# Performance work log

Hardware: AMD Instinct MI355X
Metric: run time of the kernel (lower is better)

Reference implementation:

```python
import jax, jax.numpy as jnp
import numpy as np

B, T = 64, 512
OBS, DM, DS, NL = 115, 128, 8, 3
EMB, NA, H1 = 16, 19, 256


def _ln(x, g, b, eps=1e-5):
    m = jnp.mean(x, -1, keepdims=True)
    v = jnp.mean((x - m) ** 2, -1, keepdims=True)
    return (x - m) * jax.lax.rsqrt(v + eps) * g + b


def _s6(x, h, lng, lnb, w_ig, w_dt, b_dt, a_log, w_b, w_c, d_par, w_out):
    # x: [B,T,DM], h: [B,DM,DS]
    xn = _ln(x, lng, lnb)
    xp = xn @ w_ig.T                               # [B,T,2*DM]
    x_in, z = xp[..., :DM], xp[..., DM:]
    dt = jax.nn.softplus(x_in @ w_dt.T + b_dt)     # [B,T,DM]
    A = -jnp.exp(a_log)                            # [DM,DS]
    bt = x_in @ w_b.T                              # [B,T,DS]
    ct = x_in @ w_c.T                              # [B,T,DS]
    dA = jnp.exp(dt[..., None] * A)                # [B,T,DM,DS]
    upd = (dt * x_in)[..., None] * bt[:, :, None, :]  # [B,T,DM,DS]

    def step(hc, inp):
        dA_t, u_t, c_t = inp
        hn = dA_t * hc + u_t                       # [B,DM,DS]
        y = jnp.einsum('bds,bs->bd', hn, c_t)      # [B,DM]
        return hn, y

    h_f, ys = jax.lax.scan(
        step, h,
        (jnp.swapaxes(dA, 0, 1), jnp.swapaxes(upd, 0, 1), jnp.swapaxes(ct, 0, 1)))
    y = jnp.swapaxes(ys, 0, 1)                     # [B,T,DM]
    ssm = y * jax.nn.silu(z) + x_in * d_par
    return x + ssm @ w_out.T, h_f.reshape(h_f.shape[0], -1)


def _forward(prev_actions, obs, h0, enc_w1, enc_b1, enc_g1, enc_bb1, enc_w2, enc_b2,
             enc_g2, enc_bb2, emb, proj_w, proj_b, proj_g, proj_bb,
             m_ln_g, m_ln_b, m_w_ig, m_w_dt, m_b_dt, m_a_log, m_w_b, m_w_c, m_d, m_w_out,
             fn_g, fn_b, pol_w1, pol_b1, pol_g, pol_bb, pol_w2, pol_b2):
    # MLP encoder: Linear -> LN -> SiLU -> Linear -> LN (final norm)
    e = jax.nn.silu(_ln(obs @ enc_w1.T + enc_b1, enc_g1, enc_bb1))
    e = _ln(e @ enc_w2.T + enc_b2, enc_g2, enc_bb2)
    pa = emb[prev_actions]                         # [B,T,EMB]
    x = jnp.concatenate([e, pa], -1) @ proj_w.T + proj_b
    x = jax.nn.silu(_ln(x, proj_g, proj_bb))
    for i in range(NL):
        x, _ = _s6(x, h0[i].reshape(-1, DM, DS), m_ln_g[i], m_ln_b[i], m_w_ig[i],
                   m_w_dt[i], m_b_dt[i], m_a_log[i], m_w_b[i], m_w_c[i], m_d[i], m_w_out[i])
    x = _ln(x, fn_g, fn_b)
    p = jax.nn.silu(_ln(x @ pol_w1.T + pol_b1, pol_g, pol_bb))
    return p @ pol_w2.T + pol_b2                   # [B,T,NA] policy logits


def setup_inputs() -> dict:
    key = jax.random.key(0)
    ks = iter(jax.random.split(key, 64))
    def n(shape, s=0.05):
        return jax.random.normal(next(ks), shape, dtype=jnp.float32) * s
    return {
        'obs': jax.random.normal(next(ks), (B, T, OBS), dtype=jnp.float32),
        'h0': jnp.zeros((NL, B, DM * DS), jnp.float32),
        'enc_w1': n((H1, OBS)), 'enc_b1': jnp.zeros((H1,)),
        'enc_g1': jnp.ones((H1,)), 'enc_bb1': jnp.zeros((H1,)),
        'enc_w2': n((DM, H1)), 'enc_b2': jnp.zeros((DM,)),
        'enc_g2': jnp.ones((DM,)), 'enc_bb2': jnp.zeros((DM,)),
        'emb': n((NA + 1, EMB), 1.0),
        'proj_w': n((DM, DM + EMB)), 'proj_b': jnp.zeros((DM,)),
        'proj_g': jnp.ones((DM,)), 'proj_bb': jnp.zeros((DM,)),
        'm_ln_g': jnp.ones((NL, DM)), 'm_ln_b': jnp.zeros((NL, DM)),
        'm_w_ig': n((NL, 2 * DM, DM)), 'm_w_dt': n((NL, DM, DM)),
        'm_b_dt': jnp.zeros((NL, DM)),
        'm_a_log': jax.random.uniform(next(ks), (NL, DM, DS), minval=-3.0, maxval=-1.0, dtype=jnp.float32),
        'm_w_b': n((NL, DS, DM)), 'm_w_c': n((NL, DS, DM)),
        'm_d': jnp.ones((NL, DM)), 'm_w_out': n((NL, DM, DM)),
        'fn_g': jnp.ones((DM,)), 'fn_b': jnp.zeros((DM,)),
        'pol_w1': n((DM, DM)), 'pol_b1': jnp.zeros((DM,)),
        'pol_g': jnp.ones((DM,)), 'pol_bb': jnp.zeros((DM,)),
        'pol_w2': n((NA, DM)), 'pol_b2': jnp.zeros((NA,)),
        'prev_actions': jax.random.randint(next(ks), (B, T), 0, NA + 1),
    }


def reference(obs, h0, enc_w1, enc_b1, enc_g1, enc_bb1, enc_w2, enc_b2, enc_g2, enc_bb2,
              emb, proj_w, proj_b, proj_g, proj_bb, m_ln_g, m_ln_b, m_w_ig, m_w_dt,
              m_b_dt, m_a_log, m_w_b, m_w_c, m_d, m_w_out, fn_g, fn_b, pol_w1, pol_b1,
              pol_g, pol_bb, pol_w2, pol_b2, prev_actions):
    return _forward(prev_actions, obs, h0, enc_w1, enc_b1, enc_g1, enc_bb1, enc_w2,
                    enc_b2, enc_g2, enc_bb2, emb, proj_w, proj_b, proj_g, proj_bb,
                    m_ln_g, m_ln_b, m_w_ig, m_w_dt, m_b_dt, m_a_log, m_w_b, m_w_c,
                    m_d, m_w_out, fn_g, fn_b, pol_w1, pol_b1, pol_g, pol_bb, pol_w2, pol_b2)
```

## Files before the change

### kernel.cpp

```cpp
#include <hip/hip_runtime.h>
#include <math.h>

#define BB 64
#define TT 512
#define OBSD 115
#define DMD 128
#define DSD 8
#define NLD 3
#define EMBD 16
#define NAD 19
#define H1D 256
#define NTOK (BB*TT)
#define SSEG 32
#define TSEG (TT/SSEG)

typedef unsigned short ushort_t;
typedef __attribute__((ext_vector_type(8))) short short8;
typedef __attribute__((ext_vector_type(4))) float f32x4;

__device__ __forceinline__ float silu_f(float x){ return x / (1.f + __expf(-x)); }
__device__ __forceinline__ float softplus_f(float x){
  return fmaxf(x, 0.f) + log1pf(__expf(-fabsf(x)));
}
__device__ __forceinline__ ushort_t f2bf(float x){
  unsigned u = __float_as_uint(x);
  unsigned r = (u + 0x7fffu + ((u >> 16) & 1u)) >> 16;
  return (ushort_t)r;
}
__device__ __forceinline__ float b2f(ushort_t x){
  return __uint_as_float(((unsigned)x) << 16);
}
#define MFMA(a,b,c) __builtin_amdgcn_mfma_f32_16x16x32_bf16((a),(b),(c),0,0,0)
#define LOG2E 1.44269504f

template<int D, int SV>
__device__ __forceinline__ void ln32(const float* s_val, float* s_mr, int tid){
  const int t = tid >> 3, part = tid & 7;
  float s = 0.f, s2 = 0.f;
  #pragma unroll
  for (int j = part; j < D; j += 8){ float v = s_val[t*SV + j]; s += v; s2 = fmaf(v, v, s2); }
  s += __shfl_xor(s, 1, 64); s2 += __shfl_xor(s2, 1, 64);
  s += __shfl_xor(s, 2, 64); s2 += __shfl_xor(s2, 2, 64);
  s += __shfl_xor(s, 4, 64); s2 += __shfl_xor(s2, 4, 64);
  if (part == 0){
    float m = s * (1.f/(float)D);
    s_mr[t*2] = m;
    s_mr[t*2+1] = rsqrtf(s2 * (1.f/(float)D) - m*m + 1e-5f);
  }
}

struct PJob { const float* src; ushort_t* dst; int N; int K; int Kpad; int rowofs; int Nw; };
struct PJobs { PJob j[20]; };

__global__ __launch_bounds__(256) void k_prep(PJobs P){
  const int job = blockIdx.x >> 2;
  const int sub = blockIdx.x & 3;
  PJob pj = P.j[job];
  const int elems = pj.Nw * pj.Kpad;
  for (int idx = sub*256 + threadIdx.x; idx < elems; idx += 4*256){
    int n = idx / pj.Kpad;
    int k = idx - n*pj.Kpad;
    float v = (n < pj.N && k < pj.K) ? pj.src[(size_t)n*pj.K + k] : 0.f;
    pj.dst[(size_t)(pj.rowofs + n)*pj.Kpad + k] = f2bf(v);
  }
}

__global__ __launch_bounds__(256) void k_enc1(
    const float* __restrict__ obs, const ushort_t* __restrict__ w1b,
    const float* __restrict__ b1, const float* __restrict__ g1,
    const float* __restrict__ bb1, ushort_t* __restrict__ e1)
{
  __shared__ __align__(16) char sm[34048];
  float*    s_val = (float*)sm;
  ushort_t* s_a   = (ushort_t*)sm;
  float*    s_mr  = (float*)(sm + 33792);
  const int tok0 = blockIdx.x * 32;
  const int tid = threadIdx.x;
  const int lane = tid & 63, w = tid >> 6;
  const int q = lane >> 4, cn = lane & 15;
  const int m0 = (w & 1) * 16, nh = w >> 1;

  for (int e = tid; e < 32*16; e += 256){
    int t = e >> 4, kc = e & 15;
    const float* op = obs + (size_t)(tok0 + t)*OBSD;
    short8 v;
    #pragma unroll
    for (int j = 0; j < 8; j++){
      int k = kc*8 + j;
      v[j] = (short)f2bf(k < OBSD ? op[k] : 0.f);
    }
    *(short8*)&s_a[t*136 + kc*8] = v;
  }
  __syncthreads();

  short8 af[4];
  #pragma unroll
  for (int ks = 0; ks < 4; ks++)
    af[ks] = *(const short8*)&s_a[(m0 + cn)*136 + ks*32 + q*8];
  __syncthreads();

  #pragma unroll
  for (int nt = 0; nt < 8; nt++){
    const int n0 = (nh*8 + nt) * 16;
    f32x4 acc = {0.f,0.f,0.f,0.f};
    #pragma unroll
    for (int ks = 0; ks < 4; ks++){
      short8 bf = *(const short8*)&w1b[(size_t)(n0 + cn)*128 + ks*32 + q*8];
      acc = MFMA(af[ks], bf, acc);
    }
    float bias = b1[n0 + cn];
    #pragma unroll
    for (int r = 0; r < 4; r++)
      s_val[(m0 + q*4 + r)*264 + n0 + cn] = acc[r] + bias;
  }
  __syncthreads();

  ln32<256,264>(s_val, s_mr, tid);
  __syncthreads();
  for (int e = tid; e < 32*256; e += 256){
    int t = e >> 8, c = e & 255;
    float v = (s_val[t*264 + c] - s_mr[t*2]) * s_mr[t*2+1] * g1[c] + bb1[c];
    e1[(size_t)(tok0 + t)*256 + c] = f2bf(silu_f(v));
  }
}

__global__ __launch_bounds__(256) void k_enc2p(
    const ushort_t* __restrict__ e1, const ushort_t* __restrict__ w2b,
    const float* __restrict__ b2, const float* __restrict__ g2,
    const float* __restrict__ bb2,
    const float* __restrict__ emb, const int* __restrict__ pact,
    const ushort_t* __restrict__ pwb, const float* __restrict__ pb,
    const float* __restrict__ pg, const float* __restrict__ pbb,
    float* __restrict__ X,
    const float* __restrict__ lng, const float* __restrict__ lnb,
    const ushort_t* __restrict__ wigb, const ushort_t* __restrict__ wdbcb,
    const float* __restrict__ bdt,
    ushort_t* __restrict__ XINb, ushort_t* __restrict__ Zb,
    ushort_t* __restrict__ DTb, ushort_t* __restrict__ BTu, ushort_t* __restrict__ CTu,
    const float* __restrict__ alog0,
    float* __restrict__ HLOC, float* __restrict__ PPR)
{
  __shared__ __align__(16) char sm[28928];
  float*    s_val = (float*)sm;
  ushort_t* s_xin = (ushort_t*)sm;
  ushort_t* s_dt  = (ushort_t*)(sm + 8704);
  ushort_t* s_a   = (ushort_t*)(sm + 17408);
  ushort_t* s_btc = (ushort_t*)(sm + 28160);
  float*    s_mr  = (float*)(sm + 28672);

  const int tok0 = blockIdx.x * 32;
  const int bidx = blockIdx.x >> 4;
  const int ch   = blockIdx.x & 15;
  const int tid = threadIdx.x;
  const int lane = tid & 63, w = tid >> 6;
  const int q = lane >> 4, cn = lane & 15;
  const int m0 = (w & 1) * 16, nh = w >> 1;

  for (int e = tid; e < 32*32; e += 256){
    int t = e >> 5, k = e & 31;
    float v = 0.f;
    if (k < EMBD){ int a = pact[tok0 + t]; v = emb[(size_t)a*EMBD + k]; }
    s_a[t*168 + 128 + k] = f2bf(v);
  }
  {
    short8 af[8];
    #pragma unroll
    for (int ks = 0; ks < 8; ks++)
      af[ks] = *(const short8*)&e1[(size_t)(tok0 + m0 + cn)*256 + ks*32 + q*8];
    #pragma unroll
    for (int nt = 0; nt < 4; nt++){
      const int n0 = (nh*4 + nt) * 16;
      f32x4 acc = {0.f,0.f,0.f,0.f};
      #pragma unroll
      for (int ks = 0; ks < 8; ks++){
        short8 bf = *(const short8*)&w2b[(size_t)(n0 + cn)*256 + ks*32 + q*8];
        acc = MFMA(af[ks], bf, acc);
      }
      float bias = b2[n0 + cn];
      #pragma unroll
      for (int r = 0; r < 4; r++)
        s_val[(m0 + q*4 + r)*136 + n0 + cn] = acc[r] + bias;
    }
  }
  __syncthreads();

  ln32<128,136>(s_val, s_mr, tid);
  __syncthreads();
  for (int e = tid; e < 32*128; e += 256){
    int t = e >> 7, c = e & 127;
    float v = (s_val[t*136 + c] - s_mr[t*2]) * s_mr[t*2+1] * g2[c] + bb2[c];
    s_a[t*168 + c] = f2bf(v);
  }
  __syncthreads();

  {
    short8 af2[5];
    #pragma unroll
    for (int ks = 0; ks < 5; ks++)
      af2[ks] = *(const short8*)&s_a[(m0 + cn)*168 + ks*32 + q*8];
    #pragma unroll
    for (int nt = 0; nt < 4; nt++){
      const int n0 = (nh*4 + nt) * 16;
      f32x4 acc = {0.f,0.f,0.f,0.f};
      #pragma unroll
      for (int ks = 0; ks < 5; ks++){
        short8 bf = *(const short8*)&pwb[(size_t)(n0 + cn)*160 + ks*32 + q*8];
        acc = MFMA(af2[ks], bf, acc);
      }
      float bias = pb[n0 + cn];
      #pragma unroll
      for (int r = 0; r < 4; r++)
        s_val[(m0 + q*4 + r)*136 + n0 + cn] = acc[r] + bias;
    }
  }
  __syncthreads();

  ln32<128,136>(s_val, s_mr, tid);
  __syncthreads();
  for (int e = tid; e < 32*128; e += 256){
    int t = e >> 7, c = e & 127;
    float v = (s_val[t*136 + c] - s_mr[t*2]) * s_mr[t*2+1] * pg[c] + pbb[c];
    v = silu_f(v);
    X[(size_t)tok0*128 + e] = v;
    s_val[t*136 + c] = v;
  }
  __syncthreads();

  ln32<128,136>(s_val, s_mr, tid);
  __syncthreads();
  for (int e = tid; e < 32*128; e += 256){
    int t = e >> 7, c = e & 127;
    float v = (s_val[t*136 + c] - s_mr[t*2]) * s_mr[t*2+1] * lng[c] + lnb[c];
    s_a[t*168 + c] = f2bf(v);
  }
  __syncthreads();

  {
    short8 af[4];
    #pragma unroll
    for (int ks = 0; ks < 4; ks++)
      af[ks] = *(const short8*)&s_a[(m0 + cn)*168 + ks*32 + q*8];
    #pragma unroll
    for (int nt = 0; nt < 8; nt++){
      const int n0 = (nh*8 + nt) * 16;
      f32x4 acc = {0.f,0.f,0.f,0.f};
      #pragma unroll
      for (int ks = 0; ks < 4; ks++){
        short8 bf = *(const short8*)&wigb[(size_t)(n0 + cn)*128 + ks*32 + q*8];
        acc = MFMA(af[ks], bf, acc);
      }
      if (n0 < 128){
        #pragma unroll
        for (int r = 0; r < 4; r++){
          int tr = m0 + q*4 + r;
          ushort_t bb = f2bf(acc[r]);
          XINb[(size_t)(tok0 + tr)*128 + n0 + cn] = bb;
          s_xin[tr*136 + n0 + cn] = bb;
        }
      } else {
        #pragma unroll
        for (int r = 0; r < 4; r++){
          int tr = m0 + q*4 + r;
          Zb[(size_t)(tok0 + tr)*128 + (n0 - 128) + cn] = f2bf(acc[r]);
        }
      }
    }
  }
  __syncthreads();

  {
    short8 af2[4];
    #pragma unroll
    for (int ks = 0; ks < 4; ks++)
      af2[ks] = *(const short8*)&s_xin[(m0 + cn)*136 + ks*32 + q*8];
    for (int nt = nh; nt < 9; nt += 2){
      const int n0 = nt * 16;
      f32x4 acc = {0.f,0.f,0.f,0.f};
      #pragma unroll
      for (int ks = 0; ks < 4; ks++){
        short8 bf = *(const short8*)&wdbcb[(size_t)(n0 + cn)*128 + ks*32 + q*8];
        acc = MFMA(af2[ks], bf, acc);
      }
      const int col = n0 + cn;
      if (col < 128){
        float bd = bdt[col];
        #pragma unroll
        for (int r = 0; r < 4; r++){
          int tr = m0 + q*4 + r;
          ushort_t dv = f2bf(softplus_f(acc[r] + bd));
          DTb[(size_t)(tok0 + tr)*128 + col] = dv;
          s_dt[tr*136 + col] = dv;
        }
      } else if (col < 136){
        #pragma unroll
        for (int r = 0; r < 4; r++){
          int tr = m0 + q*4 + r;
          ushort_t bb = f2bf(acc[r]);
          BTu[(size_t)(tok0 + tr)*8 + (col - 128)] = bb;
          s_btc[tr*8 + (col - 128)] = bb;
        }
      } else {
        #pragma unroll
        for (int r = 0; r < 4; r++)
          CTu[(size_t)(tok0 + m0 + q*4 + r)*8 + (col - 136)] = f2bf(acc[r]);
      }
    }
  }
  __syncthreads();

  {
    const int d = tid & 127, half = tid >> 7;
    float A2c[8], hh[8], pp[8];
    #pragma unroll
    for (int s = 0; s < 8; s++){
      A2c[s] = -__expf(alog0[d*8 + s]) * LOG2E;
      hh[s] = 0.f; pp[s] = 1.f;
    }
    const int t0 = half * 16;
    #pragma unroll 4
    for (int tt = 0; tt < 16; tt++){
      const int t = t0 + tt;
      float dt = b2f(s_dt[t*136 + d]);
      float wv = dt * b2f(s_xin[t*136 + d]);
      #pragma unroll
      for (int s = 0; s < 8; s++){
        float dA = exp2f(dt * A2c[s]);
        hh[s] = fmaf(dA, hh[s], wv * b2f(s_btc[t*8 + s]));
        pp[s] *= dA;
      }
    }
    const size_t o = ((size_t)bidx*SSEG + ch*2 + half)*1024 + d*8;
    #pragma unroll
    for (int s = 0; s < 8; s++){ HLOC[o+s] = hh[s]; PPR[o+s] = pp[s]; }
  }
}

#define SMS 13440

__device__ __forceinline__ void phaseB_post(
    const ushort_t* DTb, const ushort_t* XINb, const ushort_t* Zb,
    const ushort_t* BTu, const ushort_t* CTu,
    const float* __restrict__ alog, const float* __restrict__ h0g,
    const float* __restrict__ HLi, const float* __restrict__ PPi,
    const float* __restrict__ dpar, const ushort_t* __restrict__ woutb,
    float* __restrict__ X, char* sm, int b, int sg, int tid)
{
  ushort_t* s_dtS = (ushort_t*)sm;
  ushort_t* s_xiS = (ushort_t*)(sm + 4096);
  float*    s_x   = (float*)sm;
  ushort_t* s_a   = (ushort_t*)(sm + 8320);
  ushort_t* s_bt  = (ushort_t*)(sm + 12672);
  ushort_t* s_ct  = (ushort_t*)(sm + 12928);
  float*    s_mr  = (float*)(sm + 13184);

  const int d = tid;
  const int w = tid >> 6, lane = tid & 63, q = lane >> 4, cn = lane & 15;
  const size_t segtok = (size_t)b*TT + sg*TSEG;

  {
    const uint4* gdt = (const uint4*)(DTb + segtok*128);
    const uint4* gxi = (const uint4*)(XINb + segtok*128);
    #pragma unroll
    for (int i = 0; i < 2; i++){
      ((uint4*)s_dtS)[tid + i*128] = gdt[tid + i*128];
      ((uint4*)s_xiS)[tid + i*128] = gxi[tid + i*128];
    }
    if (tid < 64){
      ((unsigned*)s_bt)[tid] = ((const unsigned*)(BTu + segtok*8))[tid];
      ((unsigned*)s_ct)[tid] = ((const unsigned*)(CTu + segtok*8))[tid];
    }
  }
  float A2[8], h[8];
  #pragma unroll
  for (int s = 0; s < 8; s++){
    A2[s] = -__expf(alog[d*8 + s]) * LOG2E;
    h[s] = h0g[(size_t)b*1024 + d*8 + s];
  }
  for (int ch = 0; ch < sg; ch++){
    const size_t o = ((size_t)b*SSEG + ch)*1024 + d*8;
    float4 hl0 = *(const float4*)(HLi + o);
    float4 hl1 = *(const float4*)(HLi + o + 4);
    float4 pp0 = *(const float4*)(PPi + o);
    float4 pp1 = *(const float4*)(PPi + o + 4);
    h[0]=fmaf(pp0.x,h[0],hl0.x); h[1]=fmaf(pp0.y,h[1],hl0.y);
    h[2]=fmaf(pp0.z,h[2],hl0.z); h[3]=fmaf(pp0.w,h[3],hl0.w);
    h[4]=fmaf(pp1.x,h[4],hl1.x); h[5]=fmaf(pp1.y,h[5],hl1.y);
    h[6]=fmaf(pp1.z,h[6],hl1.z); h[7]=fmaf(pp1.w,h[7],hl1.w);
  }
  __syncthreads();

  #pragma unroll 4
  for (int t = 0; t < TSEG; t++){
    float dt = b2f(s_dtS[t*128 + d]);
    float xi = b2f(s_xiS[t*128 + d]);
    float wv = dt * xi;
    float y = 0.f;
    #pragma unroll
    for (int s = 0; s < 8; s++){
      float dA = exp2f(dt * A2[s]);
      h[s] = fmaf(dA, h[s], wv * b2f(s_bt[t*8 + s]));
      y = fmaf(h[s], b2f(s_ct[t*8 + s]), y);
    }
    s_a[t*136 + d] = f2bf(y);
  }
  __syncthreads();

  {
    const int c0 = (tid & 15)*8, trow = tid >> 4;
    float dpv[8];
    #pragma unroll
    for (int j = 0; j < 8; j++) dpv[j] = dpar[c0 + j];
    #pragma unroll
    for (int i = 0; i < 2; i++){
      const int t = trow + i*8;
      uint4 zb = ((const uint4*)(Zb + segtok*128))[tid + i*128];
      const ushort_t* zp = (const ushort_t*)&zb;
      #pragma unroll
      for (int j = 0; j < 8; j++){
        float y  = b2f(s_a[t*136 + c0 + j]);
        float xi = b2f(s_xiS[t*128 + c0 + j]);
        float ssm = y * silu_f(b2f(zp[j])) + xi * dpv[j];
        s_a[t*136 + c0 + j] = f2bf(ssm);
      }
    }
  }
  __syncthreads();

  {
    short8 af[4];
    #pragma unroll
    for (int ks = 0; ks < 4; ks++)
      af[ks] = *(const short8*)&s_a[cn*136 + ks*32 + q*8];
    for (int nt = w; nt < 8; nt += 2){
      const int n0 = nt * 16;
      short8 bf[4];
      #pragma unroll
      for (int ks = 0; ks < 4; ks++)
        bf[ks] = *(const short8*)&woutb[(size_t)(n0+cn)*128 + ks*32 + q*8];
      f32x4 acc = {0.f,0.f,0.f,0.f};
      #pragma unroll
      for (int ks = 0; ks < 4; ks++) acc = MFMA(af[ks], bf[ks], acc);
      #pragma unroll
      for (int r = 0; r < 4; r++){
        const int tr = q*4 + r;
        const size_t g = (segtok + tr)*128 + n0 + cn;
        float xn = X[g] + acc[r];
        X[g] = xn;
        s_x[tr*130 + n0 + cn] = xn;
      }
    }
  }
  __syncthreads();

  {
    const int t = tid >> 3, part = tid & 7;
    float s = 0.f, s2 = 0.f;
    const float* row = s_x + t*130 + part*16;
    #pragma unroll
    for (int j = 0; j < 16; j++){ float v = row[j]; s += v; s2 = fmaf(v, v, s2); }
    s  += __shfl_xor(s, 1, 64);  s2 += __shfl_xor(s2, 1, 64);
    s  += __shfl_xor(s, 2, 64);  s2 += __shfl_xor(s2, 2, 64);
    s  += __shfl_xor(s, 4, 64);  s2 += __shfl_xor(s2, 4, 64);
    if (part == 0){
      float m = s * (1.f/128.f);
      s_mr[t*2] = m;
      s_mr[t*2+1] = rsqrtf(s2 * (1.f/128.f) - m*m + 1e-5f);
    }
  }
  __syncthreads();
}

__global__ __launch_bounds__(256) void k_scan2p(
    ushort_t* DTb, ushort_t* XINb, ushort_t* Zb,
    ushort_t* BTu, ushort_t* CTu,
    const float* __restrict__ alog, const float* __restrict__ h0g,
    const float* __restrict__ HLi, const float* __restrict__ PPi,
    const float* __restrict__ dpar, const ushort_t* __restrict__ woutb,
    float* __restrict__ X,
    const float* __restrict__ lng, const float* __restrict__ lnb,
    const ushort_t* __restrict__ wigb, const ushort_t* __restrict__ wdbcb,
    const float* __restrict__ bdt,
    const float* __restrict__ alogn,
    float* __restrict__ HLo, float* __restrict__ PPo)
{
  __shared__ __align__(16) char sm_all[2*SMS];
  const int sub = threadIdx.x >> 7;
  char* sm = sm_all + sub*SMS;
  const int tid = threadIdx.x & 127;

  float*    s_x  = (float*)sm;
  ushort_t* s_xin= (ushort_t*)sm;
  ushort_t* s_a  = (ushort_t*)(sm + 8320);
  ushort_t* s_bt = (ushort_t*)(sm + 12672);
  float*    s_mr = (float*)(sm + 13184);

  const int b = blockIdx.x >> 4;
  const int sg = (blockIdx.x & 15)*2 + sub;
  const int w = tid >> 6, lane = tid & 63, q = lane >> 4, cn = lane & 15;
  const size_t segtok = (size_t)b*TT + sg*TSEG;

  phaseB_post(DTb, XINb, Zb, BTu, CTu, alog, h0g, HLi, PPi, dpar, woutb, X, sm, b, sg, tid);

  {
    float g = lng[tid], c0v = lnb[tid];
    #pragma unroll
    for (int t = 0; t < TSEG; t++){
      float v = (s_x[t*130 + tid] - s_mr[t*2]) * s_mr[t*2+1] * g + c0v;
      s_a[t*136 + tid] = f2bf(v);
    }
  }
  __syncthreads();

  {
    short8 af[4];
    #pragma unroll
    for (int ks = 0; ks < 4; ks++)
      af[ks] = *(const short8*)&s_a[cn*136 + ks*32 + q*8];
    for (int nt = w; nt < 16; nt += 2){
      const int n0 = nt * 16;
      short8 bf[4];
      #pragma unroll
      for (int ks = 0; ks < 4; ks++)
        bf[ks] = *(const short8*)&wigb[(size_t)(n0+cn)*128 + ks*32 + q*8];
      f32x4 acc = {0.f,0.f,0.f,0.f};
      #pragma unroll
      for (int ks = 0; ks < 4; ks++) acc = MFMA(af[ks], bf[ks], acc);
      if (n0 < 128){
        #pragma unroll
        for (int r = 0; r < 4; r++){
          const int tr = q*4 + r;
          ushort_t bb = f2bf(acc[r]);
          XINb[(segtok + tr)*128 + n0 + cn] = bb;
          s_xin[tr*136 + n0 + cn] = bb;
        }
      } else {
        #pragma unroll
        for (int r = 0; r < 4; r++){
          const int tr = q*4 + r;
          Zb[(segtok + tr)*128 + (n0-128) + cn] = f2bf(acc[r]);
        }
      }
    }
  }
  __syncthreads();

  {
    short8 af2[4];
    #pragma unroll
    for (int ks = 0; ks < 4; ks++)
      af2[ks] = *(const short8*)&s_xin[cn*136 + ks*32 + q*8];
    for (int nt = w; nt < 9; nt += 2){
      const int n0 = nt * 16;
      short8 bf[4];
      #pragma unroll
      for (int ks = 0; ks < 4; ks++)
        bf[ks] = *(const short8*)&wdbcb[(size_t)(n0+cn)*128 + ks*32 + q*8];
      const int col = n0 + cn;
      f32x4 acc = {0.f,0.f,0.f,0.f};
      #pragma unroll
      for (int ks = 0; ks < 4; ks++) acc = MFMA(af2[ks], bf[ks], acc);
      if (col < 128){
        float bd = bdt[col];
        #pragma unroll
        for (int r = 0; r < 4; r++){
          const int tr = q*4 + r;
          ushort_t dv = f2bf(softplus_f(acc[r] + bd));
          DTb[(segtok + tr)*128 + col] = dv;
          s_a[tr*136 + col] = dv;
        }
      } else if (col < 136){
        #pragma unroll
        for (int r = 0; r < 4; r++){
          const int tr = q*4 + r;
          ushort_t bb = f2bf(acc[r]);
          BTu[(segtok + tr)*8 + (col-128)] = bb;
          s_bt[tr*8 + (col-128)] = bb;
        }
      } else {
        #pragma unroll
        for (int r = 0; r < 4; r++)
          CTu[(segtok + q*4 + r)*8 + (col-136)] = f2bf(acc[r]);
      }
    }
  }
  __syncthreads();

  {
    float A2n[8], hh[8], pp[8];
    #pragma unroll
    for (int s = 0; s < 8; s++){
      A2n[s] = -__expf(alogn[tid*8 + s]) * LOG2E;
      hh[s] = 0.f; pp[s] = 1.f;
    }
    #pragma unroll 4
    for (int t = 0; t < TSEG; t++){
      float dt = b2f(s_a[t*136 + tid]);
      float wv = dt * b2f(s_xin[t*136 + tid]);
      #pragma unroll
      for (int s = 0; s < 8; s++){
        float dA = exp2f(dt * A2n[s]);
        hh[s] = fmaf(dA, hh[s], wv * b2f(s_bt[t*8 + s]));
        pp[s] *= dA;
      }
    }
    const size_t o = ((size_t)b*SSEG + sg)*1024 + tid*8;
    #pragma unroll
    for (int s = 0; s < 8; s++){ HLo[o+s] = hh[s]; PPo[o+s] = pp[s]; }
  }
}

__global__ __launch_bounds__(256) void k_scan2h(
    const ushort_t* DTb, const ushort_t* XINb, const ushort_t* Zb,
    const ushort_t* BTu, const ushort_t* CTu,
    const float* __restrict__ alog, const float* __restrict__ h0g,
    const float* __restrict__ HLi, const float* __restrict__ PPi,
    const float* __restrict__ dpar, const ushort_t* __restrict__ woutb,
    float* __restrict__ X,
    const float* __restrict__ fng, const float* __restrict__ fnb,
    const ushort_t* __restrict__ pw1b, const float* __restrict__ pb1,
    const float* __restrict__ pg, const float* __restrict__ pbb,
    const ushort_t* __restrict__ pw2b, const float* __restrict__ pb2,
    float* __restrict__ out)
{
  __shared__ __align__(16) char sm_all[2*SMS];
  const int sub = threadIdx.x >> 7;
  char* sm = sm_all + sub*SMS;
  const int tid = threadIdx.x & 127;

  float*    s_x  = (float*)sm;
  ushort_t* s_a  = (ushort_t*)(sm + 8320);
  float*    s_mr = (float*)(sm + 13184);

  const int b = blockIdx.x >> 4;
  const int sg = (blockIdx.x & 15)*2 + sub;
  const int w = tid >> 6, lane = tid & 63, q = lane >> 4, cn = lane & 15;
  const size_t segtok = (size_t)b*TT + sg*TSEG;

  phaseB_post((ushort_t*)DTb, (ushort_t*)XINb, (ushort_t*)Zb,
              (ushort_t*)BTu, (ushort_t*)CTu, alog, h0g, HLi, PPi,
              dpar, woutb, X, sm, b, sg, tid);

  {
    float g = fng[tid], c0v = fnb[tid];
    #pragma unroll
    for (int t = 0; t < TSEG; t++){
      float v = (s_x[t*130 + tid] - s_mr[t*2]) * s_mr[t*2+1] * g + c0v;
      s_a[t*136 + tid] = f2bf(v);
    }
  }
  __syncthreads();

  {
    short8 af[4];
    #pragma unroll
    for (int ks = 0; ks < 4; ks++)
      af[ks] = *(const short8*)&s_a[cn*136 + ks*32 + q*8];
    for (int nt = w; nt < 8; nt += 2){
      const int n0 = nt * 16;
      short8 bf[4];
      #pragma unroll
      for (int ks = 0; ks < 4; ks++)
        bf[ks] = *(const short8*)&pw1b[(size_t)(n0+cn)*128 + ks*32 + q*8];
      float bias = pb1[n0 + cn];
      f32x4 acc = {0.f,0.f,0.f,0.f};
      #pragma unroll
      for (int ks = 0; ks < 4; ks++) acc = MFMA(af[ks], bf[ks], acc);
      #pragma unroll
      for (int r = 0; r < 4; r++)
        s_x[(q*4 + r)*130 + n0 + cn] = acc[r] + bias;
    }
  }
  __syncthreads();

  {
    const int t = tid >> 3, part = tid & 7;
    float s = 0.f, s2 = 0.f;
    const float* row = s_x + t*130 + part*16;
    #pragma unroll
    for (int j = 0; j < 16; j++){ float v = row[j]; s += v; s2 = fmaf(v, v, s2); }
    s  += __shfl_xor(s, 1, 64);  s2 += __shfl_xor(s2, 1, 64);
    s  += __shfl_xor(s, 2, 64);  s2 += __shfl_xor(s2, 2, 64);
    s  += __shfl_xor(s, 4, 64);  s2 += __shfl_xor(s2, 4, 64);
    if (part == 0){
      float m = s * (1.f/128.f);
      s_mr[t*2] = m;
      s_mr[t*2+1] = rsqrtf(s2 * (1.f/128.f) - m*m + 1e-5f);
    }
  }
  __syncthreads();
  {
    float g = pg[tid], c0v = pbb[tid];
    #pragma unroll
    for (int t = 0; t < TSEG; t++){
      float v = (s_x[t*130 + tid] - s_mr[t*2]) * s_mr[t*2+1] * g + c0v;
      s_a[t*136 + tid] = f2bf(silu_f(v));
    }
  }
  __syncthreads();

  {
    short8 af[4];
    #pragma unroll
    for (int ks = 0; ks < 4; ks++)
      af[ks] = *(const short8*)&s_a[cn*136 + ks*32 + q*8];
    const int n0 = w * 16;
    short8 bf[4];
    #pragma unroll
    for (int ks = 0; ks < 4; ks++)
      bf[ks] = *(const short8*)&pw2b[(size_t)(n0+cn)*128 + ks*32 + q*8];
    const int col = n0 + cn;
    f32x4 acc = {0.f,0.f,0.f,0.f};
    #pragma unroll
    for (int ks = 0; ks < 4; ks++) acc = MFMA(af[ks], bf[ks], acc);
    if (col < NAD){
      float bias = pb2[col];
      #pragma unroll
      for (int r = 0; r < 4; r++)
        out[(segtok + q*4 + r)*NAD + col] = acc[r] + bias;
    }
  }
}

extern "C" void kernel_launch(void* const* d_in, const int* in_sizes, int n_in,
                              void* d_out, int out_size, void* d_ws, size_t ws_size,
                              hipStream_t stream) {
  const float* obs    = (const float*)d_in[0];
  const float* h0     = (const float*)d_in[1];
  const float* enc_w1 = (const float*)d_in[2];
  const float* enc_b1 = (const float*)d_in[3];
  const float* enc_g1 = (const float*)d_in[4];
  const float* enc_bb1= (const float*)d_in[5];
  const float* enc_w2 = (const float*)d_in[6];
  const float* enc_b2 = (const float*)d_in[7];
  const float* enc_g2 = (const float*)d_in[8];
  const float* enc_bb2= (const float*)d_in[9];
  const float* emb    = (const float*)d_in[10];
  const float* proj_w = (const float*)d_in[11];
  const float* proj_b = (const float*)d_in[12];
  const float* proj_g = (const float*)d_in[13];
  const float* proj_bb= (const float*)d_in[14];
  const float* m_ln_g = (const float*)d_in[15];
  const float* m_ln_b = (const float*)d_in[16];
  const float* m_w_ig = (const float*)d_in[17];
  const float* m_w_dt = (const float*)d_in[18];
  const float* m_b_dt = (const float*)d_in[19];
  const float* m_a_log= (const float*)d_in[20];
  const float* m_w_b  = (const float*)d_in[21];
  const float* m_w_c  = (const float*)d_in[22];
  const float* m_d    = (const float*)d_in[23];
  const float* m_w_out= (const float*)d_in[24];
  const float* fn_g   = (const float*)d_in[25];
  const float* fn_b   = (const float*)d_in[26];
  const float* pol_w1 = (const float*)d_in[27];
  const float* pol_b1 = (const float*)d_in[28];
  const float* pol_g  = (const float*)d_in[29];
  const float* pol_bb = (const float*)d_in[30];
  const float* pol_w2 = (const float*)d_in[31];
  const float* pol_b2 = (const float*)d_in[32];
  const int*   pact   = (const int*)d_in[33];

  float* ws  = (float*)d_ws;
  float* X    = ws;
  float* HLA  = X + (size_t)NTOK*128;
  float* PPA  = HLA + (size_t)BB*SSEG*1024;
  ushort_t* E1 = (ushort_t*)(PPA + (size_t)BB*SSEG*1024);
  float* HLB  = (float*)E1;
  float* PPB  = HLB + (size_t)BB*SSEG*1024;
  ushort_t* XINb = E1   + (size_t)NTOK*256;
  ushort_t* Zb   = XINb + (size_t)NTOK*128;
  ushort_t* DTb  = Zb   + (size_t)NTOK*128;
  ushort_t* BTu  = DTb  + (size_t)NTOK*128;
  ushort_t* CTu  = BTu  + (size_t)NTOK*8;

  ushort_t* W1B   = CTu   + (size_t)NTOK*8;
  ushort_t* W2B   = W1B   + 256*128;
  ushort_t* PWB   = W2B   + 128*256;
  ushort_t* WIGB  = PWB   + 128*160;
  ushort_t* WDBCB = WIGB  + 3*256*128;
  ushort_t* WOUTB = WDBCB + 3*144*128;
  ushort_t* PW1B  = WOUTB + 3*128*128;
  ushort_t* PW2B  = PW1B  + 128*128;

  PJobs P;
  int nj = 0;
  auto add = [&](const float* src, ushort_t* dst, int N, int K, int Kpad, int rowofs, int Nw){
    P.j[nj].src = src; P.j[nj].dst = dst; P.j[nj].N = N; P.j[nj].K = K;
    P.j[nj].Kpad = Kpad; P.j[nj].rowofs = rowofs; P.j[nj].Nw = Nw; nj++;
  };
  add(enc_w1, W1B, 256, 115, 128, 0, 256);
  add(enc_w2, W2B, 128, 256, 256, 0, 128);
  add(proj_w, PWB, 128, 144, 160, 0, 128);
  for (int l = 0; l < NLD; l++)
    add(m_w_ig + (size_t)l*256*128, WIGB + (size_t)l*256*128, 256, 128, 128, 0, 256);
  for (int l = 0; l < NLD; l++){
    add(m_w_dt + (size_t)l*128*128, WDBCB + (size_t)l*144*128, 128, 128, 128, 0,   128);
    add(m_w_b  + (size_t)l*8*128,   WDBCB + (size_t)l*144*128,   8, 128, 128, 128,   8);
    add(m_w_c  + (size_t)l*8*128,   WDBCB + (size_t)l*144*128,   8, 128, 128, 136,   8);
  }
  for (int l = 0; l < NLD; l++)
    add(m_w_out + (size_t)l*128*128, WOUTB + (size_t)l*128*128, 128, 128, 128, 0, 128);
  add(pol_w1, PW1B, 128, 128, 128, 0, 128);
  add(pol_w2, PW2B,  19, 128, 128, 0,  32);

  k_prep<<<20*4, 256, 0, stream>>>(P);
  k_enc1<<<NTOK/32, 256, 0, stream>>>(obs, W1B, enc_b1, enc_g1, enc_bb1, E1);
  k_enc2p<<<NTOK/32, 256, 0, stream>>>(E1, W2B, enc_b2, enc_g2, enc_bb2,
      emb, pact, PWB, proj_b, proj_g, proj_bb, X,
      m_ln_g, m_ln_b, WIGB, WDBCB, m_b_dt,
      XINb, Zb, DTb, BTu, CTu,
      m_a_log, HLA, PPA);

  const int scangrid = BB*SSEG/2;
  k_scan2p<<<scangrid, 256, 0, stream>>>(DTb, XINb, Zb, BTu, CTu,
      m_a_log, h0, HLA, PPA, m_d, WOUTB, X,
      m_ln_g + 128, m_ln_b + 128,
      WIGB + (size_t)256*128, WDBCB + (size_t)144*128, m_b_dt + 128,
      m_a_log + 1024, HLB, PPB);
  k_scan2p<<<scangrid, 256, 0, stream>>>(DTb, XINb, Zb, BTu, CTu,
      m_a_log + 1024, h0 + (size_t)BB*1024, HLB, PPB, m_d + 128,
      WOUTB + (size_t)128*128, X,
      m_ln_g + 256, m_ln_b + 256,
      WIGB + (size_t)2*256*128, WDBCB + (size_t)2*144*128, m_b_dt + 256,
      m_a_log + 2048, HLA, PPA);
  k_scan2h<<<scangrid, 256, 0, stream>>>(DTb, XINb, Zb, BTu, CTu,
      m_a_log + 2048, h0 + (size_t)2*BB*1024, HLA, PPA, m_d + 256,
      WOUTB + (size_t)2*128*128, X,
      fn_g, fn_b, PW1B, pol_b1, pol_g, pol_bb, PW2B, pol_b2,
      (float*)d_out);
}
```

Before: 466.8 us.

## Split chunk-carry prefix into separate kernel and process 32-token tiles per block

Moves the sequential cross-segment state carry (combining per-segment local states and decay products) out of each scan block into a small k_carry kernel that writes the prefix state in place. Before, every block redid up to 31 carry steps. Scan blocks now handle one 32-token tile with 256 threads as a single group, using 32-row MFMA tiles split across four waves instead of two independent 16-token halves. Launch bounds request 4 blocks per CU. This adds three extra kernel launches and more barriers in exchange for removing redundant carry work and larger MFMA tiles.

```diff
diff --git a/kernel.cpp b/kernel.cpp
--- a/kernel.cpp
+++ b/kernel.cpp
@@ -335,62 +335,73 @@
   }
 }
 
-#define SMS 13440
-
-__device__ __forceinline__ void phaseB_post(
+__global__ __launch_bounds__(256) void k_carry(
+    float* __restrict__ HL, const float* __restrict__ PP,
+    const float* __restrict__ h0g)
+{
+  const int idx = blockIdx.x*256 + threadIdx.x;
+  float h = h0g[idx];
+  size_t o = (size_t)(idx >> 10) * (SSEG*1024) + (idx & 1023);
+  #pragma unroll 4
+  for (int ch = 0; ch < SSEG; ch++){
+    float hl = HL[o];
+    float pp = PP[o];
+    HL[o] = h;
+    h = fmaf(pp, h, hl);
+    o += 1024;
+  }
+}
+
+#define SMB 26368
+
+__device__ __forceinline__ void phaseB32(
     const ushort_t* DTb, const ushort_t* XINb, const ushort_t* Zb,
     const ushort_t* BTu, const ushort_t* CTu,
-    const float* __restrict__ alog, const float* __restrict__ h0g,
-    const float* __restrict__ HLi, const float* __restrict__ PPi,
+    const float* __restrict__ alog, const float* __restrict__ HLpre,
     const float* __restrict__ dpar, const ushort_t* __restrict__ woutb,
-    float* __restrict__ X, char* sm, int b, int sg, int tid)
+    float* __restrict__ X, char* sm, int b, int pair, int tid)
 {
   ushort_t* s_dtS = (ushort_t*)sm;
-  ushort_t* s_xiS = (ushort_t*)(sm + 4096);
+  ushort_t* s_xiS = (ushort_t*)(sm + 8192);
   float*    s_x   = (float*)sm;
-  ushort_t* s_a   = (ushort_t*)(sm + 8320);
-  ushort_t* s_bt  = (ushort_t*)(sm + 12672);
-  ushort_t* s_ct  = (ushort_t*)(sm + 12928);
-  float*    s_mr  = (float*)(sm + 13184);
-
-  const int d = tid;
-  const int w = tid >> 6, lane = tid & 63, q = lane >> 4, cn = lane & 15;
-  const size_t segtok = (size_t)b*TT + sg*TSEG;
+  ushort_t* s_a   = (ushort_t*)(sm + 16384);
+  ushort_t* s_bt  = (ushort_t*)(sm + 25088);
+  ushort_t* s_ct  = (ushort_t*)(sm + 25600);
+  float*    s_mr  = (float*)(sm + 26112);
+
+  const int lane = tid & 63, w = tid >> 6, q = lane >> 4, cn = lane & 15;
+  const int m0 = (w & 1) * 16, nh = w >> 1;
+  const int d = tid & 127, half = tid >> 7;
+  const size_t segtok = (size_t)b*TT + pair*32;
 
   {
     const uint4* gdt = (const uint4*)(DTb + segtok*128);
     const uint4* gxi = (const uint4*)(XINb + segtok*128);
     #pragma unroll
     for (int i = 0; i < 2; i++){
-      ((uint4*)s_dtS)[tid + i*128] = gdt[tid + i*128];
-      ((uint4*)s_xiS)[tid + i*128] = gxi[tid + i*128];
-    }
-    if (tid < 64){
+      ((uint4*)s_dtS)[tid + i*256] = gdt[tid + i*256];
+      ((uint4*)s_xiS)[tid + i*256] = gxi[tid + i*256];
+    }
+    if (tid < 128){
       ((unsigned*)s_bt)[tid] = ((const unsigned*)(BTu + segtok*8))[tid];
       ((unsigned*)s_ct)[tid] = ((const unsigned*)(CTu + segtok*8))[tid];
     }
   }
   float A2[8], h[8];
-  #pragma unroll
-  for (int s = 0; s < 8; s++){
-    A2[s] = -__expf(alog[d*8 + s]) * LOG2E;
-    h[s] = h0g[(size_t)b*1024 + d*8 + s];
-  }
-  for (int ch = 0; ch < sg; ch++){
-    const size_t o = ((size_t)b*SSEG + ch)*1024 + d*8;
-    float4 hl0 = *(const float4*)(HLi + o);
-    float4 hl1 = *(const float4*)(HLi + o + 4);
-    float4 pp0 = *(const float4*)(PPi + o);
-    float4 pp1 = *(const float4*)(PPi + o + 4);
-    h[0]=fmaf(pp0.x,h[0],hl0.x); h[1]=fmaf(pp0.y,h[1],hl0.y);
-    h[2]=fmaf(pp0.z,h[2],hl0.z); h[3]=fmaf(pp0.w,h[3],hl0.w);
-    h[4]=fmaf(pp1.x,h[4],hl1.x); h[5]=fmaf(pp1.y,h[5],hl1.y);
-    h[6]=fmaf(pp1.z,h[6],hl1.z); h[7]=fmaf(pp1.w,h[7],hl1.w);
+  {
+    const size_t o = ((size_t)b*SSEG + pair*2 + half)*1024 + d*8;
+    float4 h0v = *(const float4*)(HLpre + o);
+    float4 h1v = *(const float4*)(HLpre + o + 4);
+    h[0]=h0v.x; h[1]=h0v.y; h[2]=h0v.z; h[3]=h0v.w;
+    h[4]=h1v.x; h[5]=h1v.y; h[6]=h1v.z; h[7]=h1v.w;
+    #pragma unroll
+    for (int s = 0; s < 8; s++) A2[s] = -__expf(alog[d*8 + s]) * LOG2E;
   }
   __syncthreads();
 
   #pragma unroll 4
-  for (int t = 0; t < TSEG; t++){
+  for (int tt = 0; tt < 16; tt++){
+    const int t = half*16 + tt;
     float dt = b2f(s_dtS[t*128 + d]);
     float xi = b2f(s_xiS[t*128 + d]);
     float wv = dt * xi;
@@ -412,8 +423,8 @@
     for (int j = 0; j < 8; j++) dpv[j] = dpar[c0 + j];
     #pragma unroll
     for (int i = 0; i < 2; i++){
-      const int t = trow + i*8;
-      uint4 zb = ((const uint4*)(Zb + segtok*128))[tid + i*128];
+      const int t = trow + i*16;
+      uint4 zb = ((const uint4*)(Zb + segtok*128))[tid + i*256];
       const ushort_t* zp = (const ushort_t*)&zb;
       #pragma unroll
       for (int j = 0; j < 8; j++){
@@ -430,9 +441,11 @@
     short8 af[4];
     #pragma unroll
     for (int ks = 0; ks < 4; ks++)
-      af[ks] = *(const short8*)&s_a[cn*136 + ks*32 + q*8];
-    for (int nt = w; nt < 8; nt += 2){
-      const int n0 = nt * 16;
+      af[ks] = *(const short8*)&s_a[(m0 + cn)*136 + ks*32 + q*8];
+    __syncthreads();
+    #pragma unroll
+    for (int i = 0; i < 4; i++){
+      const int n0 = (nh*4 + i) * 16;
       short8 bf[4];
       #pragma unroll
       for (int ks = 0; ks < 4; ks++)
@@ -442,7 +455,7 @@
       for (int ks = 0; ks < 4; ks++) acc = MFMA(af[ks], bf[ks], acc);
       #pragma unroll
       for (int r = 0; r < 4; r++){
-        const int tr = q*4 + r;
+        const int tr = m0 + q*4 + r;
         const size_t g = (segtok + tr)*128 + n0 + cn;
         float xn = X[g] + acc[r];
         X[g] = xn;
@@ -470,11 +483,10 @@
   __syncthreads();
 }
 
-__global__ __launch_bounds__(256) void k_scan2p(
+__global__ __launch_bounds__(256, 4) void k_scan2p(
     ushort_t* DTb, ushort_t* XINb, ushort_t* Zb,
     ushort_t* BTu, ushort_t* CTu,
-    const float* __restrict__ alog, const float* __restrict__ h0g,
-    const float* __restrict__ HLi, const float* __restrict__ PPi,
+    const float* __restrict__ alog, const float* __restrict__ HLpre,
     const float* __restrict__ dpar, const ushort_t* __restrict__ woutb,
     float* __restrict__ X,
     const float* __restrict__ lng, const float* __restrict__ lnb,
@@ -483,30 +495,34 @@
     const float* __restrict__ alogn,
     float* __restrict__ HLo, float* __restrict__ PPo)
 {
-  __shared__ __align__(16) char sm_all[2*SMS];
-  const int sub = threadIdx.x >> 7;
-  char* sm = sm_all + sub*SMS;
-  const int tid = threadIdx.x & 127;
-
-  float*    s_x  = (float*)sm;
-  ushort_t* s_xin= (ushort_t*)sm;
-  ushort_t* s_a  = (ushort_t*)(sm + 8320);
-  ushort_t* s_bt = (ushort_t*)(sm + 12672);
-  float*    s_mr = (float*)(sm + 13184);
+  __shared__ __align__(16) char sm[SMB];
+  const int tid = threadIdx.x;
+  float*    s_x   = (float*)sm;
+  ushort_t* s_xin = (ushort_t*)sm;
+  ushort_t* s_dt2 = (ushort_t*)(sm + 8704);
+  ushort_t* s_a   = (ushort_t*)(sm + 16384);
+  ushort_t* s_btc = (ushort_t*)(sm + 25088);
+  float*    s_mr  = (float*)(sm + 26112);
 
   const int b = blockIdx.x >> 4;
-  const int sg = (blockIdx.x & 15)*2 + sub;
-  const int w = tid >> 6, lane = tid & 63, q = lane >> 4, cn = lane & 15;
-  const size_t segtok = (size_t)b*TT + sg*TSEG;
-
-  phaseB_post(DTb, XINb, Zb, BTu, CTu, alog, h0g, HLi, PPi, dpar, woutb, X, sm, b, sg, tid);
-
-  {
-    float g = lng[tid], c0v = lnb[tid];
-    #pragma unroll
-    for (int t = 0; t < TSEG; t++){
-      float v = (s_x[t*130 + tid] - s_mr[t*2]) * s_mr[t*2+1] * g + c0v;
-      s_a[t*136 + tid] = f2bf(v);
+  const int pair = blockIdx.x & 15;
+  const int lane = tid & 63, w = tid >> 6, q = lane >> 4, cn = lane & 15;
+  const int m0 = (w & 1) * 16, nh = w >> 1;
+  const int d = tid & 127, half = tid >> 7;
+  const size_t segtok = (size_t)b*TT + pair*32;
+
+  phaseB32(DTb, XINb, Zb, BTu, CTu, alog, HLpre, dpar, woutb, X, sm, b, pair, tid);
+
+  {
+    float g = lng[d], c0v = lnb[d];
+    float x31 = s_x[31*130 + d];
+    __syncthreads();
+    #pragma unroll
+    for (int tt = 0; tt < 16; tt++){
+      const int t = half*16 + tt;
+      float xv = (t == 31) ? x31 : s_x[t*130 + d];
+      float v = (xv - s_mr[t*2]) * s_mr[t*2+1] * g + c0v;
+      s_a[t*136 + d] = f2bf(v);
     }
   }
   __syncthreads();
@@ -515,9 +531,10 @@
     short8 af[4];
     #pragma unroll
     for (int ks = 0; ks < 4; ks++)
-      af[ks] = *(const short8*)&s_a[cn*136 + ks*32 + q*8];
-    for (int nt = w; nt < 16; nt += 2){
-      const int n0 = nt * 16;
+      af[ks] = *(const short8*)&s_a[(m0 + cn)*136 + ks*32 + q*8];
+    #pragma unroll
+    for (int i = 0; i < 8; i++){
+      const int n0 = (nh*8 + i) * 16;
       short8 bf[4];
       #pragma unroll
       for (int ks = 0; ks < 4; ks++)
@@ -528,7 +545,7 @@
       if (n0 < 128){
         #pragma unroll
         for (int r = 0; r < 4; r++){
-          const int tr = q*4 + r;
+          const int tr = m0 + q*4 + r;
           ushort_t bb = f2bf(acc[r]);
           XINb[(segtok + tr)*128 + n0 + cn] = bb;
           s_xin[tr*136 + n0 + cn] = bb;
@@ -536,7 +553,7 @@
       } else {
         #pragma unroll
         for (int r = 0; r < 4; r++){
-          const int tr = q*4 + r;
+          const int tr = m0 + q*4 + r;
           Zb[(segtok + tr)*128 + (n0-128) + cn] = f2bf(acc[r]);
         }
       }
@@ -548,38 +565,38 @@
     short8 af2[4];
     #pragma unroll
     for (int ks = 0; ks < 4; ks++)
-      af2[ks] = *(const short8*)&s_xin[cn*136 + ks*32 + q*8];
-    for (int nt = w; nt < 9; nt += 2){
+      af2[ks] = *(const short8*)&s_xin[(m0 + cn)*136 + ks*32 + q*8];
+    for (int nt = nh; nt < 9; nt += 2){
       const int n0 = nt * 16;
       short8 bf[4];
       #pragma unroll
       for (int ks = 0; ks < 4; ks++)
         bf[ks] = *(const short8*)&wdbcb[(size_t)(n0+cn)*128 + ks*32 + q*8];
+      f32x4 acc = {0.f,0.f,0.f,0.f};
+      #pragma unroll
+      for (int ks = 0; ks < 4; ks++) acc = MFMA(af2[ks], bf[ks], acc);
       const int col = n0 + cn;
-      f32x4 acc = {0.f,0.f,0.f,0.f};
-      #pragma unroll
-      for (int ks = 0; ks < 4; ks++) acc = MFMA(af2[ks], bf[ks], acc);
       if (col < 128){
         float bd = bdt[col];
         #pragma unroll
         for (int r = 0; r < 4; r++){
-          const int tr = q*4 + r;
+          const int tr = m0 + q*4 + r;
           ushort_t dv = f2bf(softplus_f(acc[r] + bd));
           DTb[(segtok + tr)*128 + col] = dv;
-          s_a[tr*136 + col] = dv;
+          s_dt2[tr*136 + col] = dv;
         }
       } else if (col < 136){
         #pragma unroll
         for (int r = 0; r < 4; r++){
-          const int tr = q*4 + r;
+          const int tr = m0 + q*4 + r;
           ushort_t bb = f2bf(acc[r]);
           BTu[(segtok + tr)*8 + (col-128)] = bb;
-          s_bt[tr*8 + (col-128)] = bb;
+          s_btc[tr*8 + (col-128)] = bb;
         }
       } else {
         #pragma unroll
         for (int r = 0; r < 4; r++)
-          CTu[(segtok + q*4 + r)*8 + (col-136)] = f2bf(acc[r]);
+          CTu[(segtok + m0 + q*4 + r)*8 + (col-136)] = f2bf(acc[r]);
       }
     }
   }
@@ -589,31 +606,31 @@
     float A2n[8], hh[8], pp[8];
     #pragma unroll
     for (int s = 0; s < 8; s++){
-      A2n[s] = -__expf(alogn[tid*8 + s]) * LOG2E;
+      A2n[s] = -__expf(alogn[d*8 + s]) * LOG2E;
       hh[s] = 0.f; pp[s] = 1.f;
     }
     #pragma unroll 4
-    for (int t = 0; t < TSEG; t++){
-      float dt = b2f(s_a[t*136 + tid]);
-      float wv = dt * b2f(s_xin[t*136 + tid]);
+    for (int tt = 0; tt < 16; tt++){
+      const int t = half*16 + tt;
+      float dt = b2f(s_dt2[t*136 + d]);
+      float wv = dt * b2f(s_xin[t*136 + d]);
       #pragma unroll
       for (int s = 0; s < 8; s++){
         float dA = exp2f(dt * A2n[s]);
-        hh[s] = fmaf(dA, hh[s], wv * b2f(s_bt[t*8 + s]));
+        hh[s] = fmaf(dA, hh[s], wv * b2f(s_btc[t*8 + s]));
         pp[s] *= dA;
       }
     }
-    const size_t o = ((size_t)b*SSEG + sg)*1024 + tid*8;
+    const size_t o = ((size_t)b*SSEG + pair*2 + half)*1024 + d*8;
     #pragma unroll
     for (int s = 0; s < 8; s++){ HLo[o+s] = hh[s]; PPo[o+s] = pp[s]; }
   }
 }
 
-__global__ __launch_bounds__(256) void k_scan2h(
+__global__ __launch_bounds__(256, 4) void k_scan2h(
     const ushort_t* DTb, const ushort_t* XINb, const ushort_t* Zb,
     const ushort_t* BTu, const ushort_t* CTu,
-    const float* __restrict__ alog, const float* __restrict__ h0g,
-    const float* __restrict__ HLi, const float* __restrict__ PPi,
+    const float* __restrict__ alog, const float* __restrict__ HLpre,
     const float* __restrict__ dpar, const ushort_t* __restrict__ woutb,
     float* __restrict__ X,
     const float* __restrict__ fng, const float* __restrict__ fnb,
@@ -622,30 +639,33 @@
     const ushort_t* __restrict__ pw2b, const float* __restrict__ pb2,
     float* __restrict__ out)
 {
-  __shared__ __align__(16) char sm_all[2*SMS];
-  const int sub = threadIdx.x >> 7;
-  char* sm = sm_all + sub*SMS;
-  const int tid = threadIdx.x & 127;
-
+  __shared__ __align__(16) char sm[SMB];
+  const int tid = threadIdx.x;
   float*    s_x  = (float*)sm;
-  ushort_t* s_a  = (ushort_t*)(sm + 8320);
-  float*    s_mr = (float*)(sm + 13184);
+  ushort_t* s_a  = (ushort_t*)(sm + 16384);
+  float*    s_mr = (float*)(sm + 26112);
 
   const int b = blockIdx.x >> 4;
-  const int sg = (blockIdx.x & 15)*2 + sub;
-  const int w = tid >> 6, lane = tid & 63, q = lane >> 4, cn = lane & 15;
-  const size_t segtok = (size_t)b*TT + sg*TSEG;
-
-  phaseB_post((ushort_t*)DTb, (ushort_t*)XINb, (ushort_t*)Zb,
-              (ushort_t*)BTu, (ushort_t*)CTu, alog, h0g, HLi, PPi,
-              dpar, woutb, X, sm, b, sg, tid);
-
-  {
-    float g = fng[tid], c0v = fnb[tid];
-    #pragma unroll
-    for (int t = 0; t < TSEG; t++){
-      float v = (s_x[t*130 + tid] - s_mr[t*2]) * s_mr[t*2+1] * g + c0v;
-      s_a[t*136 + tid] = f2bf(v);
+  const int pair = blockIdx.x & 15;
+  const int lane = tid & 63, w = tid >> 6, q = lane >> 4, cn = lane & 15;
+  const int m0 = (w & 1) * 16, nh = w >> 1;
+  const int d = tid & 127, half = tid >> 7;
+  const size_t segtok = (size_t)b*TT + pair*32;
+
+  phaseB32((ushort_t*)DTb, (ushort_t*)XINb, (ushort_t*)Zb,
+           (ushort_t*)BTu, (ushort_t*)CTu, alog, HLpre,
+           dpar, woutb, X, sm, b, pair, tid);
+
+  {
+    float g = fng[d], c0v = fnb[d];
+    float x31 = s_x[31*130 + d];
+    __syncthreads();
+    #pragma unroll
+    for (int tt = 0; tt < 16; tt++){
+      const int t = half*16 + tt;
+      float xv = (t == 31) ? x31 : s_x[t*130 + d];
+      float v = (xv - s_mr[t*2]) * s_mr[t*2+1] * g + c0v;
+      s_a[t*136 + d] = f2bf(v);
     }
   }
   __syncthreads();
@@ -654,9 +674,11 @@
     short8 af[4];
     #pragma unroll
     for (int ks = 0; ks < 4; ks++)
-      af[ks] = *(const short8*)&s_a[cn*136 + ks*32 + q*8];
-    for (int nt = w; nt < 8; nt += 2){
-      const int n0 = nt * 16;
+      af[ks] = *(const short8*)&s_a[(m0 + cn)*136 + ks*32 + q*8];
+    __syncthreads();
+    #pragma unroll
+    for (int i = 0; i < 4; i++){
+      const int n0 = (nh*4 + i) * 16;
       short8 bf[4];
       #pragma unroll
       for (int ks = 0; ks < 4; ks++)
@@ -667,7 +689,7 @@
       for (int ks = 0; ks < 4; ks++) acc = MFMA(af[ks], bf[ks], acc);
       #pragma unroll
       for (int r = 0; r < 4; r++)
-        s_x[(q*4 + r)*130 + n0 + cn] = acc[r] + bias;
+        s_x[(m0 + q*4 + r)*130 + n0 + cn] = acc[r] + bias;
     }
   }
   __syncthreads();
@@ -688,12 +710,17 @@
     }
   }
   __syncthreads();
-  {
-    float g = pg[tid], c0v = pbb[tid];
-    #pragma unroll
-    for (int t = 0; t < TSEG; t++){
-      float v = (s_x[t*130 + tid] - s_mr[t*2]) * s_mr[t*2+1] * g + c0v;
-      s_a[t*136 + tid] = f2bf(silu_f(v));
+
+  {
+    float g = pg[d], c0v = pbb[d];
+    float x31 = s_x[31*130 + d];
+    __syncthreads();
+    #pragma unroll
+    for (int tt = 0; tt < 16; tt++){
+      const int t = half*16 + tt;
+      float xv = (t == 31) ? x31 : s_x[t*130 + d];
+      float v = (xv - s_mr[t*2]) * s_mr[t*2+1] * g + c0v;
+      s_a[t*136 + d] = f2bf(silu_f(v));
     }
   }
   __syncthreads();
@@ -702,8 +729,8 @@
     short8 af[4];
     #pragma unroll
     for (int ks = 0; ks < 4; ks++)
-      af[ks] = *(const short8*)&s_a[cn*136 + ks*32 + q*8];
-    const int n0 = w * 16;
+      af[ks] = *(const short8*)&s_a[(m0 + cn)*136 + ks*32 + q*8];
+    const int n0 = (w >> 1) * 16;
     short8 bf[4];
     #pragma unroll
     for (int ks = 0; ks < 4; ks++)
@@ -716,7 +743,7 @@
       float bias = pb2[col];
       #pragma unroll
       for (int r = 0; r < 4; r++)
-        out[(segtok + q*4 + r)*NAD + col] = acc[r] + bias;
+        out[(segtok + m0 + q*4 + r)*NAD + col] = acc[r] + bias;
     }
   }
 }
@@ -810,21 +837,24 @@
       XINb, Zb, DTb, BTu, CTu,
       m_a_log, HLA, PPA);
 
-  const int scangrid = BB*SSEG/2;
+  const int carrygrid = BB*1024/256;
+  const int scangrid  = NTOK/32;
+
+  k_carry<<<carrygrid, 256, 0, stream>>>(HLA, PPA, h0);
   k_scan2p<<<scangrid, 256, 0, stream>>>(DTb, XINb, Zb, BTu, CTu,
-      m_a_log, h0, HLA, PPA, m_d, WOUTB, X,
+      m_a_log, HLA, m_d, WOUTB, X,
       m_ln_g + 128, m_ln_b + 128,
       WIGB + (size_t)256*128, WDBCB + (size_t)144*128, m_b_dt + 128,
       m_a_log + 1024, HLB, PPB);
+  k_carry<<<carrygrid, 256, 0, stream>>>(HLB, PPB, h0 + (size_t)BB*1024);
   k_scan2p<<<scangrid, 256, 0, stream>>>(DTb, XINb, Zb, BTu, CTu,
-      m_a_log + 1024, h0 + (size_t)BB*1024, HLB, PPB, m_d + 128,
-      WOUTB + (size_t)128*128, X,
+      m_a_log + 1024, HLB, m_d + 128, WOUTB + (size_t)128*128, X,
       m_ln_g + 256, m_ln_b + 256,
       WIGB + (size_t)2*256*128, WDBCB + (size_t)2*144*128, m_b_dt + 256,
       m_a_log + 2048, HLA, PPA);
+  k_carry<<<carrygrid, 256, 0, stream>>>(HLA, PPA, h0 + (size_t)2*BB*1024);
   k_scan2h<<<scangrid, 256, 0, stream>>>(DTb, XINb, Zb, BTu, CTu,
-      m_a_log + 2048, h0 + (size_t)2*BB*1024, HLA, PPA, m_d + 256,
-      WOUTB + (size_t)2*128*128, X,
+      m_a_log + 2048, HLA, m_d + 256, WOUTB + (size_t)2*128*128, X,
       fn_g, fn_b, PW1B, pol_b1, pol_g, pol_bb, PW2B, pol_b2,
       (float*)d_out);
 }
```

Measured after the change: 421.8 us. 9.6% less time.
